# Performance work log

Measured on AMD Instinct MI355X. Metric: run time of the kernel, lower is better.

Reference implementation:

```python
import jax, jax.numpy as jnp
import numpy as np

B, NI, NO = 4, 256, 256          # batch, num_in, num_out
DIN, DQ, DH, DOUT = 256, 256, 256, 256


def setup_inputs() -> dict:
    key = jax.random.key(0)
    ks = jax.random.split(key, 6)
    def w(k, shape, fan_in):
        return jax.random.normal(k, shape, jnp.float32) / np.sqrt(fan_in).astype(np.float32)
    return {
        "x": jax.random.normal(ks[0], (B, NI, DIN), jnp.float32),
        "query": jax.random.normal(ks[1], (B, NO, DQ), jnp.float32),
        # pre_cond_mlp: Linear(DIN -> DH)
        "W_pre": w(ks[2], (DIN, DH), DIN), "b_pre": jnp.zeros((DH,), jnp.float32),
        # cond_embed: Linear(DQ -> DH)
        "W_emb": w(ks[3], (DQ, DH), DQ), "b_emb": jnp.zeros((DH,), jnp.float32),
        # post_cond_mlp: Linear(2*DH -> DH) + GELU + Linear(DH -> DOUT)
        "W1": w(ks[4], (2 * DH, DH), 2 * DH), "b1": jnp.zeros((DH,), jnp.float32),
        "W2": w(ks[5], (DH, DOUT), DH), "b2": jnp.zeros((DOUT,), jnp.float32),
    }


def reference(x, query, W_pre, b_pre, W_emb, b_emb, W1, b1, W2, b2):
    # pre_cond_mlp(x): [B, NI, DH]
    xp = x @ W_pre + b_pre
    # cond_embed(query): [B, NO, DH]
    c = query @ W_emb + b_emb
    # Original torch code: repeat xp over NO, c over NI, concat -> [B,NI,NO,2*DH],
    # then Linear(2*DH->DH). Algebraically identical (and far cheaper) to split W1
    # and broadcast-add the two projections:
    W1x, W1c = W1[:DH], W1[DH:]          # [DH, DH] each
    h = (xp @ W1x)[:, :, None, :] + (c @ W1c)[:, None, :, :] + b1  # [B, NI, NO, DH]
    h = jax.nn.gelu(h, approximate=False)  # torch nn.GELU default = exact erf
    return h @ W2 + b2                     # [B, NI, NO, DOUT]
```

## Files before the change

### kernel.cpp

```cpp
#include <hip/hip_runtime.h>
#include <hip/hip_bf16.h>
#include <cstdint>
#include <cstddef>


typedef __bf16  bf16x8 __attribute__((ext_vector_type(8)));
typedef float   f32x16 __attribute__((ext_vector_type(16)));

__device__ __forceinline__ float fast_gelu(float x) {
    const float x2 = x * x;
    const float m  = __builtin_fmaf(x2, -0.1029433f, -2.3022072f);
    const float e  = __builtin_amdgcn_exp2f(x * m);
    return x * __builtin_amdgcn_rcpf(1.0f + e);
}

__global__ __launch_bounds__(256) void prep_kernel(
    const float* __restrict__ x, const float* __restrict__ query,
    const float* __restrict__ W_pre, const float* __restrict__ b_pre,
    const float* __restrict__ W_emb, const float* __restrict__ b_emb,
    const float* __restrict__ W1, const float* __restrict__ b1,
    const float* __restrict__ W2,
    float* __restrict__ u, float* __restrict__ v,
    unsigned short* __restrict__ w2t)
{
    const int b = blockIdx.x;
    const int t = threadIdx.x;

    if (b >= 512) {
        const int n0 = (b - 512) * 4;
        const float4 wv = *reinterpret_cast<const float4*>(W2 + (size_t)t * 256 + n0);
        const float vals[4] = {wv.x, wv.y, wv.z, wv.w};
#pragma unroll
        for (int j = 0; j < 4; ++j) {
            const __bf16 bv = (__bf16)vals[j];
            w2t[(size_t)(n0 + j) * 256 + t] = __builtin_bit_cast(unsigned short, bv);
        }
        return;
    }

    const bool isq = (b >= 256);
    const float* __restrict__ A   = isq ? query : x;
    const float* __restrict__ Wa  = isq ? W_emb : W_pre;
    const float* __restrict__ ba  = isq ? b_emb : b_pre;
    const float* __restrict__ W1p = isq ? (W1 + 256 * 256) : W1;
    float* __restrict__ outp      = isq ? v : u;
    const int r0 = (isq ? (b - 256) : b) * 4;

    __shared__ float as[4][256];
    __shared__ float xs[4][256];

#pragma unroll
    for (int r = 0; r < 4; ++r)
        as[r][t] = A[(size_t)(r0 + r) * 256 + t];
    __syncthreads();

    float acc[4] = {0.f, 0.f, 0.f, 0.f};
    {
        float wcur[8];
#pragma unroll
        for (int q = 0; q < 8; ++q) wcur[q] = Wa[(size_t)q * 256 + t];
        for (int k0 = 0; k0 < 248; k0 += 8) {
            float wnxt[8];
#pragma unroll
            for (int q = 0; q < 8; ++q)
                wnxt[q] = Wa[(size_t)(k0 + 8 + q) * 256 + t];
#pragma unroll
            for (int q = 0; q < 8; ++q)
#pragma unroll
                for (int r = 0; r < 4; ++r)
                    acc[r] = __builtin_fmaf(as[r][k0 + q], wcur[q], acc[r]);
#pragma unroll
            for (int q = 0; q < 8; ++q) wcur[q] = wnxt[q];
        }
#pragma unroll
        for (int q = 0; q < 8; ++q)
#pragma unroll
            for (int r = 0; r < 4; ++r)
                acc[r] = __builtin_fmaf(as[r][248 + q], wcur[q], acc[r]);
    }
    const float bav = ba[t];
#pragma unroll
    for (int r = 0; r < 4; ++r) xs[r][t] = acc[r] + bav;
    __syncthreads();

    float acc2[4] = {0.f, 0.f, 0.f, 0.f};
    {
        float wcur[8];
#pragma unroll
        for (int q = 0; q < 8; ++q) wcur[q] = W1p[(size_t)q * 256 + t];
        for (int k0 = 0; k0 < 248; k0 += 8) {
            float wnxt[8];
#pragma unroll
            for (int q = 0; q < 8; ++q)
                wnxt[q] = W1p[(size_t)(k0 + 8 + q) * 256 + t];
#pragma unroll
            for (int q = 0; q < 8; ++q)
#pragma unroll
                for (int r = 0; r < 4; ++r)
                    acc2[r] = __builtin_fmaf(xs[r][k0 + q], wcur[q], acc2[r]);
#pragma unroll
            for (int q = 0; q < 8; ++q) wcur[q] = wnxt[q];
        }
#pragma unroll
        for (int q = 0; q < 8; ++q)
#pragma unroll
            for (int r = 0; r < 4; ++r)
                acc2[r] = __builtin_fmaf(xs[r][248 + q], wcur[q], acc2[r]);
    }
    const float b1v = isq ? 0.f : b1[t];
#pragma unroll
    for (int r = 0; r < 4; ++r)
        outp[(size_t)(r0 + r) * 256 + t] = acc2[r] + b1v;
}

__global__ __launch_bounds__(256, 2) void fused_kernel(
    const float* __restrict__ U, const float* __restrict__ V,
    const unsigned short* __restrict__ W2T, const float* __restrict__ b2,
    float* __restrict__ out)
{
    __shared__ uint4 wlds[2048];
    __shared__ uint4 hlds[1024];
    unsigned int* const hlds32 = reinterpret_cast<unsigned int*>(hlds);

    const int t    = threadIdx.x;
    const int lane = t & 63;
    const int w    = t >> 6;
    const int l31  = lane & 31;
    const int hi   = lane >> 5;

    const size_t r0 = (size_t)blockIdx.x * 128;
    const int bb = (int)(r0 >> 16);
    const int ii = (int)((r0 >> 8) & 255);
    const int j0 = (int)(r0 & 255);

    const float* __restrict__ urow  = U + ((size_t)(bb * 256 + ii)) * 256;
    const float* __restrict__ vbase = V + ((size_t)(bb * 256 + j0)) * 256;

    f32x16 acc[8];
#pragma unroll
    for (int i = 0; i < 8; ++i) acc[i] = (f32x16)0.f;

    for (int kk = 0; kk < 256; kk += 64) {
#pragma unroll
        for (int it = 0; it < 8; ++it) {
            const int idx = it * 256 + t;
            const int n   = idx >> 3;
            const int gp  = idx & 7;
            const int g   = gp ^ (n & 7);
            __builtin_amdgcn_global_load_lds(
                (const __attribute__((address_space(1))) unsigned int*)
                    (W2T + (size_t)n * 256 + kk + g * 8),
                (__attribute__((address_space(3))) unsigned int*)
                    (wlds + idx),
                16, 0, 0);
        }

        const float2 uv2 = *reinterpret_cast<const float2*>(urow + kk + 2 * l31);
        float2 vv[16];
#pragma unroll
        for (int p = 0; p < 16; ++p) {
            const int row = w * 32 + p * 2 + hi;
            vv[p] = *reinterpret_cast<const float2*>(vbase + (size_t)row * 256 + kk + 2 * l31);
        }
#pragma unroll
        for (int p = 0; p < 16; ++p) {
            const int row = w * 32 + p * 2 + hi;
            union { unsigned int u32; __bf16 h[2]; } pk;
            pk.h[0] = (__bf16)fast_gelu(uv2.x + vv[p].x);
            pk.h[1] = (__bf16)fast_gelu(uv2.y + vv[p].y);
            const int d = l31;
            hlds32[row * 32 + (((d >> 2) ^ (row & 7)) << 2) + (d & 3)] = pk.u32;
        }
        __syncthreads();

#pragma unroll
        for (int s = 0; s < 4; ++s) {
            const int gk = 2 * s + hi;
            const int arow = w * 32 + l31;
            const bf16x8 afrag = __builtin_bit_cast(
                bf16x8, hlds[arow * 8 + (gk ^ (arow & 7))]);
#pragma unroll
            for (int cg = 0; cg < 8; ++cg) {
                const int col = cg * 32 + l31;
                const bf16x8 bfrag = __builtin_bit_cast(
                    bf16x8, wlds[col * 8 + (gk ^ (col & 7))]);
                acc[cg] = __builtin_amdgcn_mfma_f32_32x32x16_bf16(
                    afrag, bfrag, acc[cg], 0, 0, 0);
            }
        }
        __syncthreads();
    }

#pragma unroll
    for (int cg = 0; cg < 8; ++cg) {
        const int col = cg * 32 + l31;
        const float bv = b2[col];
#pragma unroll
        for (int rr = 0; rr < 16; ++rr) {
            const int row = w * 32 + 4 * hi + (rr & 3) + 8 * (rr >> 2);
            __builtin_nontemporal_store(acc[cg][rr] + bv,
                                        out + (r0 + row) * 256 + col);
        }
    }
}

extern "C" void kernel_launch(void* const* d_in, const int* in_sizes, int n_in,
                              void* d_out, int out_size, void* d_ws, size_t ws_size,
                              hipStream_t stream)
{
    const float* x     = (const float*)d_in[0];
    const float* query = (const float*)d_in[1];
    const float* W_pre = (const float*)d_in[2];
    const float* b_pre = (const float*)d_in[3];
    const float* W_emb = (const float*)d_in[4];
    const float* b_emb = (const float*)d_in[5];
    const float* W1    = (const float*)d_in[6];
    const float* b1    = (const float*)d_in[7];
    const float* W2    = (const float*)d_in[8];
    const float* b2    = (const float*)d_in[9];
    float* out = (float*)d_out;

    char* ws = (char*)d_ws;
    float* u            = (float*)(ws);
    float* v            = (float*)(ws + (1 << 20));
    unsigned short* w2t = (unsigned short*)(ws + 2 * (1 << 20));

    prep_kernel<<<576, 256, 0, stream>>>(x, query, W_pre, b_pre, W_emb, b_emb,
                                         W1, b1, W2, u, v, w2t);
    fused_kernel<<<2048, 256, 0, stream>>>(u, v, w2t, b2, out);
}
```

Baseline: 105.1 us.

## Keep GELU A-fragments in registers and stream W2 column tiles double-buffered

Restructures the fused kernel so each block computes all 256 k of the GELU activations first and holds them as 16 bf16 fragments in registers. It then loops over 8 output column groups, streaming a 32-column W2 slice per group into a double-buffered LDS tile that is prefetched while the MFMAs run. W2 is prepacked in a k-group-major layout to match this order. Accumulators shrink from 8 f32x16 to one, which allows launch bounds of 3 blocks per SM and cuts LDS use. In exchange there are per-group syncthreads, and the output stores become regular rather than nontemporal.

```diff
diff --git a/kernel.cpp b/kernel.cpp
--- a/kernel.cpp
+++ b/kernel.cpp
@@ -21,7 +21,7 @@
     const float* __restrict__ W1, const float* __restrict__ b1,
     const float* __restrict__ W2,
     float* __restrict__ u, float* __restrict__ v,
-    unsigned short* __restrict__ w2t)
+    unsigned short* __restrict__ w2f)
 {
     const int b = blockIdx.x;
     const int t = threadIdx.x;
@@ -30,10 +30,12 @@
         const int n0 = (b - 512) * 4;
         const float4 wv = *reinterpret_cast<const float4*>(W2 + (size_t)t * 256 + n0);
         const float vals[4] = {wv.x, wv.y, wv.z, wv.w};
+        const int g = t >> 3, e = t & 7;
 #pragma unroll
         for (int j = 0; j < 4; ++j) {
             const __bf16 bv = (__bf16)vals[j];
-            w2t[(size_t)(n0 + j) * 256 + t] = __builtin_bit_cast(unsigned short, bv);
+            w2f[((size_t)(g * 256 + n0 + j)) * 8 + e] =
+                __builtin_bit_cast(unsigned short, bv);
         }
         return;
     }
@@ -113,14 +115,14 @@
         outp[(size_t)(r0 + r) * 256 + t] = acc2[r] + b1v;
 }
 
-__global__ __launch_bounds__(256, 2) void fused_kernel(
+__global__ __launch_bounds__(256, 3) void fused_kernel(
     const float* __restrict__ U, const float* __restrict__ V,
-    const unsigned short* __restrict__ W2T, const float* __restrict__ b2,
+    const unsigned short* __restrict__ W2F, const float* __restrict__ b2,
     float* __restrict__ out)
 {
-    __shared__ uint4 wlds[2048];
     __shared__ uint4 hlds[1024];
-    unsigned int* const hlds32 = reinterpret_cast<unsigned int*>(hlds);
+    __shared__ uint4 blds[2][1024];
+    unsigned int* const h32 = reinterpret_cast<unsigned int*>(hlds);
 
     const int t    = threadIdx.x;
     const int lane = t & 63;
@@ -128,79 +130,90 @@
     const int l31  = lane & 31;
     const int hi   = lane >> 5;
 
-    const size_t r0 = (size_t)blockIdx.x * 128;
-    const int bb = (int)(r0 >> 16);
-    const int ii = (int)((r0 >> 8) & 255);
-    const int j0 = (int)(r0 & 255);
-
-    const float* __restrict__ urow  = U + ((size_t)(bb * 256 + ii)) * 256;
-    const float* __restrict__ vbase = V + ((size_t)(bb * 256 + j0)) * 256;
-
-    f32x16 acc[8];
-#pragma unroll
-    for (int i = 0; i < 8; ++i) acc[i] = (f32x16)0.f;
-
-    for (int kk = 0; kk < 256; kk += 64) {
-#pragma unroll
-        for (int it = 0; it < 8; ++it) {
+    const int bid  = blockIdx.x;
+    const int tile = bid >> 1;
+    const int jh   = bid & 1;
+    const int bb   = tile >> 8;
+
+    const float* __restrict__ urow  = U + (size_t)tile * 256;
+    const float* __restrict__ vbase = V + ((size_t)(bb * 256 + jh * 128)) * 256;
+
+    const int d  = t & 31;
+    const int rb = t >> 5;
+
+    auto stage_b = [&](int cg, int buf) {
+#pragma unroll
+        for (int it = 0; it < 4; ++it) {
             const int idx = it * 256 + t;
-            const int n   = idx >> 3;
-            const int gp  = idx & 7;
-            const int g   = gp ^ (n & 7);
+            const int g   = idx >> 5;
+            const int c   = idx & 31;
             __builtin_amdgcn_global_load_lds(
                 (const __attribute__((address_space(1))) unsigned int*)
-                    (W2T + (size_t)n * 256 + kk + g * 8),
+                    (W2F + ((size_t)(g * 256 + cg * 32 + c)) * 8),
                 (__attribute__((address_space(3))) unsigned int*)
-                    (wlds + idx),
+                    (&blds[buf][idx]),
                 16, 0, 0);
         }
-
-        const float2 uv2 = *reinterpret_cast<const float2*>(urow + kk + 2 * l31);
+    };
+
+    stage_b(0, 0);
+
+    bf16x8 af[16];
+#pragma unroll
+    for (int c = 0; c < 4; ++c) {
+        const int kk = c * 64;
+        const float2 u2 = *reinterpret_cast<const float2*>(urow + kk + 2 * d);
         float2 vv[16];
 #pragma unroll
         for (int p = 0; p < 16; ++p) {
-            const int row = w * 32 + p * 2 + hi;
-            vv[p] = *reinterpret_cast<const float2*>(vbase + (size_t)row * 256 + kk + 2 * l31);
+            const int row = rb + p * 8;
+            vv[p] = *reinterpret_cast<const float2*>(
+                vbase + (size_t)row * 256 + kk + 2 * d);
         }
 #pragma unroll
         for (int p = 0; p < 16; ++p) {
-            const int row = w * 32 + p * 2 + hi;
+            const int row = rb + p * 8;
             union { unsigned int u32; __bf16 h[2]; } pk;
-            pk.h[0] = (__bf16)fast_gelu(uv2.x + vv[p].x);
-            pk.h[1] = (__bf16)fast_gelu(uv2.y + vv[p].y);
-            const int d = l31;
-            hlds32[row * 32 + (((d >> 2) ^ (row & 7)) << 2) + (d & 3)] = pk.u32;
+            pk.h[0] = (__bf16)fast_gelu(u2.x + vv[p].x);
+            pk.h[1] = (__bf16)fast_gelu(u2.y + vv[p].y);
+            h32[row * 32 + (((d >> 2) ^ (row & 7)) << 2) + (d & 3)] = pk.u32;
         }
         __syncthreads();
-
+        const int arow = w * 32 + l31;
 #pragma unroll
         for (int s = 0; s < 4; ++s) {
-            const int gk = 2 * s + hi;
-            const int arow = w * 32 + l31;
-            const bf16x8 afrag = __builtin_bit_cast(
-                bf16x8, hlds[arow * 8 + (gk ^ (arow & 7))]);
-#pragma unroll
-            for (int cg = 0; cg < 8; ++cg) {
-                const int col = cg * 32 + l31;
-                const bf16x8 bfrag = __builtin_bit_cast(
-                    bf16x8, wlds[col * 8 + (gk ^ (col & 7))]);
-                acc[cg] = __builtin_amdgcn_mfma_f32_32x32x16_bf16(
-                    afrag, bfrag, acc[cg], 0, 0, 0);
-            }
+            const int gl = 2 * s + hi;
+            af[c * 4 + s] = __builtin_bit_cast(
+                bf16x8, hlds[arow * 8 + (gl ^ (arow & 7))]);
         }
         __syncthreads();
     }
 
+    float bvv[8];
+#pragma unroll
+    for (int cg = 0; cg < 8; ++cg) bvv[cg] = b2[cg * 32 + l31];
+
+    const size_t obase = ((size_t)tile << 16) + (size_t)(jh * 128 + w * 32) * 256;
+
 #pragma unroll
     for (int cg = 0; cg < 8; ++cg) {
+        if (cg < 7) stage_b(cg + 1, (cg + 1) & 1);
+
+        f32x16 acc = (f32x16)0.f;
+#pragma unroll
+        for (int S = 0; S < 16; ++S) {
+            const bf16x8 bf_ = __builtin_bit_cast(
+                bf16x8, blds[cg & 1][(2 * S + hi) * 32 + l31]);
+            acc = __builtin_amdgcn_mfma_f32_32x32x16_bf16(af[S], bf_, acc, 0, 0, 0);
+        }
+
         const int col = cg * 32 + l31;
-        const float bv = b2[col];
 #pragma unroll
         for (int rr = 0; rr < 16; ++rr) {
-            const int row = w * 32 + 4 * hi + (rr & 3) + 8 * (rr >> 2);
-            __builtin_nontemporal_store(acc[cg][rr] + bv,
-                                        out + (r0 + row) * 256 + col);
-        }
+            const int row = 4 * hi + (rr & 3) + 8 * (rr >> 2);
+            out[obase + (size_t)row * 256 + col] = acc[rr] + bvv[cg];
+        }
+        __syncthreads();
     }
 }
 
@@ -223,9 +236,9 @@
     char* ws = (char*)d_ws;
     float* u            = (float*)(ws);
     float* v            = (float*)(ws + (1 << 20));
-    unsigned short* w2t = (unsigned short*)(ws + 2 * (1 << 20));
+    unsigned short* w2f = (unsigned short*)(ws + 2 * (1 << 20));
 
     prep_kernel<<<576, 256, 0, stream>>>(x, query, W_pre, b_pre, W_emb, b_emb,
-                                         W1, b1, W2, u, v, w2t);
-    fused_kernel<<<2048, 256, 0, stream>>>(u, v, w2t, b2, out);
-}
+                                         W1, b1, W2, u, v, w2f);
+    fused_kernel<<<2048, 256, 0, stream>>>(u, v, w2f, b2, out);
+}
```

Result: faster. 90.66 us (median of 4 runs) (-13.7%).
